# Kernel optimization log

Hardware: AMD Instinct MI355X
Metric: run time of the kernel (lower is better)

The kernel has to match this reference:

```python
import jax, jax.numpy as jnp
import numpy as np

B, T_OBS, T_FUT, D, H = 8192, 128, 64, 5, 128


def _gru_step(h, x, Wih, Whh, bih, bhh):
    # PyTorch GRU math, gate order (r, z, n) in the stacked [3H, *] weights.
    gi = x @ Wih.T + bih          # [B, 3H]
    gh = h @ Whh.T + bhh          # [B, 3H]
    ir, iz, inn = jnp.split(gi, 3, axis=-1)
    hr, hz, hn = jnp.split(gh, 3, axis=-1)
    r = jax.nn.sigmoid(ir + hr)
    z = jax.nn.sigmoid(iz + hz)
    n = jnp.tanh(inn + r * hn)
    return (1.0 - z) * n + z * h


def setup_inputs() -> dict:
    key = jax.random.key(0)
    ks = jax.random.split(key, 12)
    s = 0.1  # modest init scale to keep gates in a sane range
    return {
        "obs": jax.random.normal(ks[0], (B, T_OBS, D), jnp.float32),
        "target": jax.random.normal(ks[1], (B, T_FUT, D), jnp.float32),
        "enc_Wih": jax.random.normal(ks[2], (3 * H, D), jnp.float32) * s,
        "enc_Whh": jax.random.normal(ks[3], (3 * H, H), jnp.float32) * s,
        "enc_bih": jax.random.normal(ks[4], (3 * H,), jnp.float32) * s,
        "enc_bhh": jax.random.normal(ks[5], (3 * H,), jnp.float32) * s,
        "cell_Wih": jax.random.normal(ks[6], (3 * H, D), jnp.float32) * s,
        "cell_Whh": jax.random.normal(ks[7], (3 * H, H), jnp.float32) * s,
        "cell_bih": jax.random.normal(ks[8], (3 * H,), jnp.float32) * s,
        "cell_bhh": jax.random.normal(ks[9], (3 * H,), jnp.float32) * s,
        "head_W": jax.random.normal(ks[10], (D, H), jnp.float32) * s,
        "head_b": jax.random.normal(ks[11], (D,), jnp.float32) * s,
    }


def reference(obs, target, enc_Wih, enc_Whh, enc_bih, enc_bhh,
              cell_Wih, cell_Whh, cell_bih, cell_bhh, head_W, head_b):
    b = obs.shape[0]
    h0 = jnp.zeros((b, H), obs.dtype)

    # --- encoder: GRU over obs, keep only final hidden state ---
    def enc_step(h, x):
        h_new = _gru_step(h, x, enc_Wih, enc_Whh, enc_bih, enc_bhh)
        return h_new, None
    hT, _ = jax.lax.scan(enc_step, h0, jnp.swapaxes(obs, 0, 1))  # xs: [T_obs, B, D]

    # --- teacher-forced rollout: x_0 = obs[:, -1], x_t = target[:, t-1] ---
    xs = jnp.concatenate([obs[:, -1:, :], target[:, :-1, :]], axis=1)  # [B, T_fut, D]
    def roll_step(h, x):
        h_new = _gru_step(h, x, cell_Wih, cell_Whh, cell_bih, cell_bhh)
        return h_new, h_new
    _, hs = jax.lax.scan(roll_step, hT, jnp.swapaxes(xs, 0, 1))  # hs: [T_fut, B, H]

    preds = jnp.einsum('tbh,dh->tbd', hs, head_W) + head_b  # [T_fut, B, D]
    return jnp.swapaxes(preds, 0, 1)  # [B, T_fut, D]
```

## Files before the change

kernel.cpp:

```cpp
#include <hip/hip_runtime.h>

#define B_TOT 8192
#define T_OBS 128
#define T_FUT 64
#define T_ALL 192
#define DIN 5
#define HD 128
#define BT 32
#define LDSTR 136

#define LOG2E 1.44269504088896340736f

typedef __attribute__((ext_vector_type(8))) short short8;
typedef __attribute__((ext_vector_type(4))) float f32x4;
typedef __attribute__((ext_vector_type(2))) unsigned int u32x2;
typedef __attribute__((ext_vector_type(4))) unsigned int u32x4;

__device__ inline short f2bf(float f) {
    unsigned u = __float_as_uint(f);
    u += 0x7FFFu + ((u >> 16) & 1u);
    return (short)(u >> 16);
}

__device__ inline unsigned cvtpk(float lo, float hi) {
    unsigned r;
    asm volatile("v_cvt_pk_bf16_f32 %0, %1, %2" : "=v"(r) : "v"(lo), "v"(hi));
    return r;
}

__device__ inline f32x4 MFMA(short8 a, short8 b, f32x4 c) {
    return __builtin_amdgcn_mfma_f32_16x16x32_bf16(a, b, c, 0, 0, 0);
}

__device__ inline short8 load_w8s(const float* p, float s) {
    float4 a = *reinterpret_cast<const float4*>(p);
    float4 b = *reinterpret_cast<const float4*>(p + 4);
    short8 r;
    r[0] = f2bf(a.x * s); r[1] = f2bf(a.y * s); r[2] = f2bf(a.z * s); r[3] = f2bf(a.w * s);
    r[4] = f2bf(b.x * s); r[5] = f2bf(b.y * s); r[6] = f2bf(b.z * s); r[7] = f2bf(b.w * s);
    return r;
}
__device__ inline short8 load_w5s(const float* p, float s) {
    short8 r = (short8)0;
    r[0] = f2bf(p[0] * s); r[1] = f2bf(p[1] * s); r[2] = f2bf(p[2] * s);
    r[3] = f2bf(p[3] * s); r[4] = f2bf(p[4] * s);
    return r;
}

__global__ __launch_bounds__(512, 1)
void gru_tracemodel_kernel(const float* __restrict__ obs, const float* __restrict__ target,
                           const float* __restrict__ eWih, const float* __restrict__ eWhh,
                           const float* __restrict__ ebih, const float* __restrict__ ebhh,
                           const float* __restrict__ cWih, const float* __restrict__ cWhh,
                           const float* __restrict__ cbih, const float* __restrict__ cbhh,
                           const float* __restrict__ headW, const float* __restrict__ headb,
                           float* __restrict__ out)
{
    __shared__ __attribute__((aligned(16))) short Abuf[2][BT][LDSTR];

    const int tid   = threadIdx.x;
    const int wave  = tid >> 6;
    const int lane  = tid & 63;
    const int q     = lane >> 4;
    const int c     = lane & 15;
    const int b0    = blockIdx.x * BT;
    const int wbase = wave * 16;

    for (int i = tid; i < 2 * BT * LDSTR; i += 512) ((short*)Abuf)[i] = 0;

    short8 Wr[5], Wz[5], Wn[5];
    f32x4  br4, bz4, bnh4, bni4;

    auto load_phase = [&](const float* Wih, const float* Whh,
                          const float* bih, const float* bhh) {
        const int nr = 0 * HD + wbase + c;
        const int nz = 1 * HD + wbase + c;
        const int nn = 2 * HD + wbase + c;
        #pragma unroll
        for (int kt = 0; kt < 4; ++kt) {
            Wr[kt] = load_w8s(Whh + nr * HD + kt * 32 + q * 8, LOG2E);
            Wz[kt] = load_w8s(Whh + nz * HD + kt * 32 + q * 8, LOG2E);
            Wn[kt] = load_w8s(Whh + nn * HD + kt * 32 + q * 8, 2.f * LOG2E);
        }
        Wr[4] = (q == 0) ? load_w5s(Wih + nr * DIN, LOG2E) : (short8)0;
        Wz[4] = (q == 0) ? load_w5s(Wih + nz * DIN, LOG2E) : (short8)0;
        Wn[4] = (q == 0) ? load_w5s(Wih + nn * DIN, 2.f * LOG2E) : (short8)0;
        const int n0 = wbase + q * 4;
        #pragma unroll
        for (int r = 0; r < 4; ++r) {
            br4[r]  = (bih[0 * HD + n0 + r] + bhh[0 * HD + n0 + r]) * LOG2E;
            bz4[r]  = (bih[1 * HD + n0 + r] + bhh[1 * HD + n0 + r]) * LOG2E;
            bni4[r] = bih[2 * HD + n0 + r] * (2.f * LOG2E);
            bnh4[r] = bhh[2 * HD + n0 + r] * (2.f * LOG2E);
        }
    };
    load_phase(eWih, eWhh, ebih, ebhh);

    short8 Whd[4];
    f32x4  hb4;
    #pragma unroll
    for (int kt = 0; kt < 4; ++kt)
        Whd[kt] = (c < DIN) ? load_w8s(headW + c * HD + kt * 32 + q * 8, 1.f) : (short8)0;
    #pragma unroll
    for (int r = 0; r < 4; ++r)
        hb4[r] = (q * 4 + r < DIN) ? headb[q * 4 + r] : 0.f;

    float hreg[2][4] = {{0.f,0.f,0.f,0.f},{0.f,0.f,0.f,0.f}};

    const float* obsr[2] = { obs + (size_t)(b0 + c) * (T_OBS * DIN),
                             obs + (size_t)(b0 + 16 + c) * (T_OBS * DIN) };
    const float* tgtr[2] = { target + (size_t)(b0 + c) * (T_FUT * DIN),
                             target + (size_t)(b0 + 16 + c) * (T_FUT * DIN) };
    float x5[2][5] = {{0,0,0,0,0},{0,0,0,0,0}};
    if (q == 0) {
        #pragma unroll
        for (int a = 0; a < 2; ++a) {
            float4 v4 = *reinterpret_cast<const float4*>(obsr[a]);
            x5[a][0] = v4.x; x5[a][1] = v4.y; x5[a][2] = v4.z; x5[a][3] = v4.w;
            x5[a][4] = obsr[a][4];
        }
    }

#define GRU_STEP(T, DO_HEAD, ENC)                                              \
  {                                                                            \
    __syncthreads();                                                           \
    const int p_ = (T) & 1;                                                    \
    short8 ah[2][4];                                                           \
    _Pragma("unroll")                                                          \
    for (int a = 0; a < 2; ++a) {                                              \
      const short* ap = &Abuf[p_][a * 16 + c][0];                              \
      _Pragma("unroll")                                                        \
      for (int kt = 0; kt < 4; ++kt)                                           \
        ah[a][kt] = *reinterpret_cast<const short8*>(ap + kt * 32 + q * 8);    \
    }                                                                          \
    if (DO_HEAD) {                                                             \
      const int s_ = (T) - (T_OBS + 1);                                        \
      if (wave == (s_ & 7)) {                                                  \
        const int d0 = q * 4;                                                  \
        _Pragma("unroll")                                                      \
        for (int a = 0; a < 2; ++a) {                                          \
          f32x4 acc = hb4;                                                     \
          _Pragma("unroll")                                                    \
          for (int kt = 0; kt < 4; ++kt)                                       \
            acc = MFMA(Whd[kt], ah[a][kt], acc);                               \
          if (d0 < DIN) {                                                      \
            float* op = out + ((size_t)(b0 + a * 16 + c) * T_FUT + s_) * DIN + d0; \
            op[0] = acc[0];                                                    \
            if (q == 0) { op[1] = acc[1]; op[2] = acc[2]; op[3] = acc[3]; }    \
          }                                                                    \
        }                                                                      \
      }                                                                        \
    }                                                                          \
    short8 ax[2];                                                              \
    {                                                                          \
      u32x4 va = { cvtpk(x5[0][0], x5[0][1]), cvtpk(x5[0][2], x5[0][3]),       \
                   cvtpk(x5[0][4], 0.f), 0u };                                 \
      u32x4 vb = { cvtpk(x5[1][0], x5[1][1]), cvtpk(x5[1][2], x5[1][3]),       \
                   cvtpk(x5[1][4], 0.f), 0u };                                 \
      ax[0] = __builtin_bit_cast(short8, va);                                  \
      ax[1] = __builtin_bit_cast(short8, vb);                                  \
      if (q == 0) {                                                            \
        const int tn_ = (T) + 1;                                               \
        _Pragma("unroll")                                                      \
        for (int a = 0; a < 2; ++a) {                                          \
          const float* px = (ENC)                                              \
              ? (obsr[a] + ((tn_ < T_OBS) ? tn_ : (T_OBS - 1)) * DIN)          \
              : (tgtr[a] + (tn_ - T_OBS - 1) * DIN);                           \
          float4 v4 = *reinterpret_cast<const float4*>(px);                    \
          x5[a][0] = v4.x; x5[a][1] = v4.y; x5[a][2] = v4.z; x5[a][3] = v4.w;  \
          x5[a][4] = px[4];                                                    \
        }                                                                      \
      }                                                                        \
    }                                                                          \
    _Pragma("unroll")                                                          \
    for (int a = 0; a < 2; ++a) {                                              \
      f32x4 aR  = MFMA(Wr[0], ah[a][0], br4);                                  \
      f32x4 aZ  = MFMA(Wz[0], ah[a][0], bz4);                                  \
      f32x4 aNh = MFMA(Wn[0], ah[a][0], bnh4);                                 \
      _Pragma("unroll")                                                        \
      for (int kt = 1; kt < 4; ++kt) {                                         \
        aR  = MFMA(Wr[kt], ah[a][kt], aR);                                     \
        aZ  = MFMA(Wz[kt], ah[a][kt], aZ);                                     \
        aNh = MFMA(Wn[kt], ah[a][kt], aNh);                                    \
      }                                                                        \
      aR  = MFMA(Wr[4], ax[a], aR);                                            \
      aZ  = MFMA(Wz[4], ax[a], aZ);                                            \
      f32x4 aNi = MFMA(Wn[4], ax[a], bni4);                                    \
      float hn[4];                                                             \
      _Pragma("unroll")                                                        \
      for (int r = 0; r < 4; ++r) {                                            \
        float er  = __builtin_amdgcn_exp2f(-aR[r]);                            \
        float rv  = __builtin_amdgcn_rcpf(1.f + er);                           \
        float yv  = fmaf(rv, aNh[r], aNi[r]);                                  \
        float ey  = __builtin_amdgcn_exp2f(yv);                                \
        float ez  = __builtin_amdgcn_exp2f(-aZ[r]);                            \
        float d2  = 1.f + ey;                                                  \
        float d1  = 1.f + ez;                                                  \
        float em1 = ey - 1.f;                                                  \
        float num = fmaf(ez, em1, hreg[a][r] * d2);                            \
        float h_  = num * __builtin_amdgcn_rcpf(d1 * d2);                      \
        hreg[a][r] = h_;                                                       \
        hn[r] = h_;                                                            \
      }                                                                        \
      u32x2 wv = { cvtpk(hn[0], hn[1]), cvtpk(hn[2], hn[3]) };                 \
      *reinterpret_cast<u32x2*>(&Abuf[1 - p_][a * 16 + c][wbase + q * 4]) = wv;\
    }                                                                          \
  }

    for (int t = 0; t < T_OBS; ++t) GRU_STEP(t, 0, 1);

    load_phase(cWih, cWhh, cbih, cbhh);
    GRU_STEP(T_OBS, 0, 0);

    for (int t = T_OBS + 1; t < T_ALL; ++t) GRU_STEP(t, 1, 0);

    __syncthreads();
    if (wave == ((T_FUT - 1) & 7)) {
        const int p_ = T_ALL & 1;
        const int s_ = T_FUT - 1;
        const int d0 = q * 4;
        #pragma unroll
        for (int a = 0; a < 2; ++a) {
            const short* ap = &Abuf[p_][a * 16 + c][0];
            f32x4 acc = hb4;
            #pragma unroll
            for (int kt = 0; kt < 4; ++kt) {
                short8 h8 = *reinterpret_cast<const short8*>(ap + kt * 32 + q * 8);
                acc = MFMA(Whd[kt], h8, acc);
            }
            if (d0 < DIN) {
                float* op = out + ((size_t)(b0 + a * 16 + c) * T_FUT + s_) * DIN + d0;
                op[0] = acc[0];
                if (q == 0) { op[1] = acc[1]; op[2] = acc[2]; op[3] = acc[3]; }
            }
        }
    }
#undef GRU_STEP
}

extern "C" void kernel_launch(void* const* d_in, const int* in_sizes, int n_in,
                              void* d_out, int out_size, void* d_ws, size_t ws_size,
                              hipStream_t stream)
{
    (void)in_sizes; (void)n_in; (void)d_ws; (void)ws_size; (void)out_size;
    gru_tracemodel_kernel<<<dim3(B_TOT / BT), dim3(512), 0, stream>>>(
        (const float*)d_in[0],  (const float*)d_in[1],
        (const float*)d_in[2],  (const float*)d_in[3],
        (const float*)d_in[4],  (const float*)d_in[5],
        (const float*)d_in[6],  (const float*)d_in[7],
        (const float*)d_in[8],  (const float*)d_in[9],
        (const float*)d_in[10], (const float*)d_in[11],
        (float*)d_out);
}
```

Measured before the change: 322.5 us.

## Halve batch tile to 16 with 4 waves each owning 32 hidden units

Restructures the work split so each block handles 16 batch rows using 256 threads (4 waves), with each wave computing two 16-wide hidden-unit groups instead of two batch halves. This doubles the grid to 512 blocks and allows two blocks per CU, meant to improve latency hiding across the sequential recurrence and reduce barrier cost per block. The head weights move from registers into LDS to relieve register pressure for the doubled per-wave gate weights. The trade-off is that each thread now holds twice as many weight fragments in registers.

```diff
diff --git a/kernel.cpp b/kernel.cpp
--- a/kernel.cpp
+++ b/kernel.cpp
@@ -6,8 +6,9 @@
 #define T_ALL 192
 #define DIN 5
 #define HD 128
-#define BT 32
+#define BT 16
 #define LDSTR 136
+#define NTHR 256
 
 #define LOG2E 1.44269504088896340736f
 
@@ -47,7 +48,7 @@
     return r;
 }
 
-__global__ __launch_bounds__(512, 1)
+__global__ __launch_bounds__(NTHR, 2)
 void gru_tracemodel_kernel(const float* __restrict__ obs, const float* __restrict__ target,
                            const float* __restrict__ eWih, const float* __restrict__ eWhh,
                            const float* __restrict__ ebih, const float* __restrict__ ebhh,
@@ -57,135 +58,132 @@
                            float* __restrict__ out)
 {
     __shared__ __attribute__((aligned(16))) short Abuf[2][BT][LDSTR];
-
-    const int tid   = threadIdx.x;
-    const int wave  = tid >> 6;
-    const int lane  = tid & 63;
-    const int q     = lane >> 4;
-    const int c     = lane & 15;
-    const int b0    = blockIdx.x * BT;
-    const int wbase = wave * 16;
-
-    for (int i = tid; i < 2 * BT * LDSTR; i += 512) ((short*)Abuf)[i] = 0;
-
-    short8 Wr[5], Wz[5], Wn[5];
-    f32x4  br4, bz4, bnh4, bni4;
+    __shared__ __attribute__((aligned(16))) short Hw[DIN][LDSTR];
+    __shared__ float HbLds[8];
+
+    const int tid  = threadIdx.x;
+    const int wave = tid >> 6;
+    const int lane = tid & 63;
+    const int q    = lane >> 4;
+    const int c    = lane & 15;
+    const int b0   = blockIdx.x * BT;
+    const int wb0  = wave * 32;
+
+    for (int i = tid; i < 2 * BT * LDSTR; i += NTHR) ((short*)Abuf)[i] = 0;
+
+    short8 Wr[2][5], Wz[2][5], Wn[2][5];
+    f32x4  br4[2], bz4[2], bnh4[2], bni4[2];
 
     auto load_phase = [&](const float* Wih, const float* Whh,
                           const float* bih, const float* bhh) {
-        const int nr = 0 * HD + wbase + c;
-        const int nz = 1 * HD + wbase + c;
-        const int nn = 2 * HD + wbase + c;
+        #pragma unroll
+        for (int g = 0; g < 2; ++g) {
+            const int nr = 0 * HD + wb0 + 16 * g + c;
+            const int nz = 1 * HD + wb0 + 16 * g + c;
+            const int nn = 2 * HD + wb0 + 16 * g + c;
+            #pragma unroll
+            for (int kt = 0; kt < 4; ++kt) {
+                Wr[g][kt] = load_w8s(Whh + nr * HD + kt * 32 + q * 8, LOG2E);
+                Wz[g][kt] = load_w8s(Whh + nz * HD + kt * 32 + q * 8, LOG2E);
+                Wn[g][kt] = load_w8s(Whh + nn * HD + kt * 32 + q * 8, 2.f * LOG2E);
+            }
+            Wr[g][4] = (q == 0) ? load_w5s(Wih + nr * DIN, LOG2E) : (short8)0;
+            Wz[g][4] = (q == 0) ? load_w5s(Wih + nz * DIN, LOG2E) : (short8)0;
+            Wn[g][4] = (q == 0) ? load_w5s(Wih + nn * DIN, 2.f * LOG2E) : (short8)0;
+            const int n0 = wb0 + 16 * g + q * 4;
+            #pragma unroll
+            for (int r = 0; r < 4; ++r) {
+                br4[g][r]  = (bih[0 * HD + n0 + r] + bhh[0 * HD + n0 + r]) * LOG2E;
+                bz4[g][r]  = (bih[1 * HD + n0 + r] + bhh[1 * HD + n0 + r]) * LOG2E;
+                bni4[g][r] = bih[2 * HD + n0 + r] * (2.f * LOG2E);
+                bnh4[g][r] = bhh[2 * HD + n0 + r] * (2.f * LOG2E);
+            }
+        }
+    };
+    load_phase(eWih, eWhh, ebih, ebhh);
+
+    if (wave == 0 && c < DIN) {
         #pragma unroll
         for (int kt = 0; kt < 4; ++kt) {
-            Wr[kt] = load_w8s(Whh + nr * HD + kt * 32 + q * 8, LOG2E);
-            Wz[kt] = load_w8s(Whh + nz * HD + kt * 32 + q * 8, LOG2E);
-            Wn[kt] = load_w8s(Whh + nn * HD + kt * 32 + q * 8, 2.f * LOG2E);
-        }
-        Wr[4] = (q == 0) ? load_w5s(Wih + nr * DIN, LOG2E) : (short8)0;
-        Wz[4] = (q == 0) ? load_w5s(Wih + nz * DIN, LOG2E) : (short8)0;
-        Wn[4] = (q == 0) ? load_w5s(Wih + nn * DIN, 2.f * LOG2E) : (short8)0;
-        const int n0 = wbase + q * 4;
-        #pragma unroll
-        for (int r = 0; r < 4; ++r) {
-            br4[r]  = (bih[0 * HD + n0 + r] + bhh[0 * HD + n0 + r]) * LOG2E;
-            bz4[r]  = (bih[1 * HD + n0 + r] + bhh[1 * HD + n0 + r]) * LOG2E;
-            bni4[r] = bih[2 * HD + n0 + r] * (2.f * LOG2E);
-            bnh4[r] = bhh[2 * HD + n0 + r] * (2.f * LOG2E);
-        }
-    };
-    load_phase(eWih, eWhh, ebih, ebhh);
-
-    short8 Whd[4];
-    f32x4  hb4;
-    #pragma unroll
-    for (int kt = 0; kt < 4; ++kt)
-        Whd[kt] = (c < DIN) ? load_w8s(headW + c * HD + kt * 32 + q * 8, 1.f) : (short8)0;
-    #pragma unroll
-    for (int r = 0; r < 4; ++r)
-        hb4[r] = (q * 4 + r < DIN) ? headb[q * 4 + r] : 0.f;
+            short8 w = load_w8s(headW + c * HD + kt * 32 + q * 8, 1.f);
+            *reinterpret_cast<short8*>(&Hw[c][kt * 32 + q * 8]) = w;
+        }
+    }
+    if (tid < 8) HbLds[tid] = (tid < DIN) ? headb[tid] : 0.f;
 
     float hreg[2][4] = {{0.f,0.f,0.f,0.f},{0.f,0.f,0.f,0.f}};
 
-    const float* obsr[2] = { obs + (size_t)(b0 + c) * (T_OBS * DIN),
-                             obs + (size_t)(b0 + 16 + c) * (T_OBS * DIN) };
-    const float* tgtr[2] = { target + (size_t)(b0 + c) * (T_FUT * DIN),
-                             target + (size_t)(b0 + 16 + c) * (T_FUT * DIN) };
-    float x5[2][5] = {{0,0,0,0,0},{0,0,0,0,0}};
+    const float* obsr = obs    + (size_t)(b0 + c) * (T_OBS * DIN);
+    const float* tgtr = target + (size_t)(b0 + c) * (T_FUT * DIN);
+    float x5[5] = {0, 0, 0, 0, 0};
     if (q == 0) {
-        #pragma unroll
-        for (int a = 0; a < 2; ++a) {
-            float4 v4 = *reinterpret_cast<const float4*>(obsr[a]);
-            x5[a][0] = v4.x; x5[a][1] = v4.y; x5[a][2] = v4.z; x5[a][3] = v4.w;
-            x5[a][4] = obsr[a][4];
-        }
+        float4 v4 = *reinterpret_cast<const float4*>(obsr);
+        x5[0] = v4.x; x5[1] = v4.y; x5[2] = v4.z; x5[3] = v4.w;
+        x5[4] = obsr[4];
     }
 
 #define GRU_STEP(T, DO_HEAD, ENC)                                              \
   {                                                                            \
     __syncthreads();                                                           \
     const int p_ = (T) & 1;                                                    \
-    short8 ah[2][4];                                                           \
-    _Pragma("unroll")                                                          \
-    for (int a = 0; a < 2; ++a) {                                              \
-      const short* ap = &Abuf[p_][a * 16 + c][0];                              \
+    short8 ah[4];                                                              \
+    {                                                                          \
+      const short* ap = &Abuf[p_][c][0];                                       \
       _Pragma("unroll")                                                        \
       for (int kt = 0; kt < 4; ++kt)                                           \
-        ah[a][kt] = *reinterpret_cast<const short8*>(ap + kt * 32 + q * 8);    \
+        ah[kt] = *reinterpret_cast<const short8*>(ap + kt * 32 + q * 8);       \
     }                                                                          \
     if (DO_HEAD) {                                                             \
       const int s_ = (T) - (T_OBS + 1);                                        \
-      if (wave == (s_ & 7)) {                                                  \
+      if (wave == (s_ & 3)) {                                                  \
+        const short* hwp = &Hw[(c < DIN) ? c : 0][0];                          \
+        f32x4 acc = {0.f, 0.f, 0.f, 0.f};                                      \
+        _Pragma("unroll")                                                      \
+        for (int kt = 0; kt < 4; ++kt) {                                       \
+          short8 wh = *reinterpret_cast<const short8*>(hwp + kt * 32 + q * 8); \
+          acc = MFMA(wh, ah[kt], acc);                                         \
+        }                                                                      \
         const int d0 = q * 4;                                                  \
-        _Pragma("unroll")                                                      \
-        for (int a = 0; a < 2; ++a) {                                          \
-          f32x4 acc = hb4;                                                     \
-          _Pragma("unroll")                                                    \
-          for (int kt = 0; kt < 4; ++kt)                                       \
-            acc = MFMA(Whd[kt], ah[a][kt], acc);                               \
-          if (d0 < DIN) {                                                      \
-            float* op = out + ((size_t)(b0 + a * 16 + c) * T_FUT + s_) * DIN + d0; \
-            op[0] = acc[0];                                                    \
-            if (q == 0) { op[1] = acc[1]; op[2] = acc[2]; op[3] = acc[3]; }    \
+        if (d0 < DIN) {                                                        \
+          float* op = out + ((size_t)(b0 + c) * T_FUT + s_) * DIN + d0;        \
+          op[0] = acc[0] + HbLds[d0];                                          \
+          if (q == 0) {                                                        \
+            op[1] = acc[1] + HbLds[1];                                         \
+            op[2] = acc[2] + HbLds[2];                                         \
+            op[3] = acc[3] + HbLds[3];                                         \
           }                                                                    \
         }                                                                      \
       }                                                                        \
     }                                                                          \
-    short8 ax[2];                                                              \
+    short8 ax;                                                                 \
     {                                                                          \
-      u32x4 va = { cvtpk(x5[0][0], x5[0][1]), cvtpk(x5[0][2], x5[0][3]),       \
-                   cvtpk(x5[0][4], 0.f), 0u };                                 \
-      u32x4 vb = { cvtpk(x5[1][0], x5[1][1]), cvtpk(x5[1][2], x5[1][3]),       \
-                   cvtpk(x5[1][4], 0.f), 0u };                                 \
-      ax[0] = __builtin_bit_cast(short8, va);                                  \
-      ax[1] = __builtin_bit_cast(short8, vb);                                  \
+      u32x4 va = { cvtpk(x5[0], x5[1]), cvtpk(x5[2], x5[3]),                   \
+                   cvtpk(x5[4], 0.f), 0u };                                    \
+      ax = __builtin_bit_cast(short8, va);                                     \
       if (q == 0) {                                                            \
         const int tn_ = (T) + 1;                                               \
-        _Pragma("unroll")                                                      \
-        for (int a = 0; a < 2; ++a) {                                          \
-          const float* px = (ENC)                                              \
-              ? (obsr[a] + ((tn_ < T_OBS) ? tn_ : (T_OBS - 1)) * DIN)          \
-              : (tgtr[a] + (tn_ - T_OBS - 1) * DIN);                           \
-          float4 v4 = *reinterpret_cast<const float4*>(px);                    \
-          x5[a][0] = v4.x; x5[a][1] = v4.y; x5[a][2] = v4.z; x5[a][3] = v4.w;  \
-          x5[a][4] = px[4];                                                    \
-        }                                                                      \
+        const float* px = (ENC)                                                \
+            ? (obsr + ((tn_ < T_OBS) ? tn_ : (T_OBS - 1)) * DIN)               \
+            : (tgtr + (tn_ - T_OBS - 1) * DIN);                                \
+        float4 v4 = *reinterpret_cast<const float4*>(px);                      \
+        x5[0] = v4.x; x5[1] = v4.y; x5[2] = v4.z; x5[3] = v4.w;                \
+        x5[4] = px[4];                                                         \
       }                                                                        \
     }                                                                          \
     _Pragma("unroll")                                                          \
-    for (int a = 0; a < 2; ++a) {                                              \
-      f32x4 aR  = MFMA(Wr[0], ah[a][0], br4);                                  \
-      f32x4 aZ  = MFMA(Wz[0], ah[a][0], bz4);                                  \
-      f32x4 aNh = MFMA(Wn[0], ah[a][0], bnh4);                                 \
+    for (int g = 0; g < 2; ++g) {                                              \
+      f32x4 aR  = MFMA(Wr[g][0], ah[0], br4[g]);                               \
+      f32x4 aZ  = MFMA(Wz[g][0], ah[0], bz4[g]);                               \
+      f32x4 aNh = MFMA(Wn[g][0], ah[0], bnh4[g]);                              \
       _Pragma("unroll")                                                        \
       for (int kt = 1; kt < 4; ++kt) {                                         \
-        aR  = MFMA(Wr[kt], ah[a][kt], aR);                                     \
-        aZ  = MFMA(Wz[kt], ah[a][kt], aZ);                                     \
-        aNh = MFMA(Wn[kt], ah[a][kt], aNh);                                    \
-      }                                                                        \
-      aR  = MFMA(Wr[4], ax[a], aR);                                            \
-      aZ  = MFMA(Wz[4], ax[a], aZ);                                            \
-      f32x4 aNi = MFMA(Wn[4], ax[a], bni4);                                    \
+        aR  = MFMA(Wr[g][kt], ah[kt], aR);                                     \
+        aZ  = MFMA(Wz[g][kt], ah[kt], aZ);                                     \
+        aNh = MFMA(Wn[g][kt], ah[kt], aNh);                                    \
+      }                                                                        \
+      aR  = MFMA(Wr[g][4], ax, aR);                                            \
+      aZ  = MFMA(Wz[g][4], ax, aZ);                                            \
+      f32x4 aNi = MFMA(Wn[g][4], ax, bni4[g]);                                 \
       float hn[4];                                                             \
       _Pragma("unroll")                                                        \
       for (int r = 0; r < 4; ++r) {                                            \
@@ -197,13 +195,14 @@
         float d2  = 1.f + ey;                                                  \
         float d1  = 1.f + ez;                                                  \
         float em1 = ey - 1.f;                                                  \
-        float num = fmaf(ez, em1, hreg[a][r] * d2);                            \
+        float num = fmaf(ez, em1, hreg[g][r] * d2);                            \
         float h_  = num * __builtin_amdgcn_rcpf(d1 * d2);                      \
-        hreg[a][r] = h_;                                                       \
+        hreg[g][r] = h_;                                                       \
         hn[r] = h_;                                                            \
       }                                                                        \
       u32x2 wv = { cvtpk(hn[0], hn[1]), cvtpk(hn[2], hn[3]) };                 \
-      *reinterpret_cast<u32x2*>(&Abuf[1 - p_][a * 16 + c][wbase + q * 4]) = wv;\
+      *reinterpret_cast<u32x2*>(                                               \
+          &Abuf[1 - p_][c][wb0 + 16 * g + q * 4]) = wv;                        \
     }                                                                          \
   }
 
@@ -215,23 +214,26 @@
     for (int t = T_OBS + 1; t < T_ALL; ++t) GRU_STEP(t, 1, 0);
 
     __syncthreads();
-    if (wave == ((T_FUT - 1) & 7)) {
+    if (wave == ((T_FUT - 1) & 3)) {
         const int p_ = T_ALL & 1;
         const int s_ = T_FUT - 1;
         const int d0 = q * 4;
+        const short* ap  = &Abuf[p_][c][0];
+        const short* hwp = &Hw[(c < DIN) ? c : 0][0];
+        f32x4 acc = {0.f, 0.f, 0.f, 0.f};
         #pragma unroll
-        for (int a = 0; a < 2; ++a) {
-            const short* ap = &Abuf[p_][a * 16 + c][0];
-            f32x4 acc = hb4;
-            #pragma unroll
-            for (int kt = 0; kt < 4; ++kt) {
-                short8 h8 = *reinterpret_cast<const short8*>(ap + kt * 32 + q * 8);
-                acc = MFMA(Whd[kt], h8, acc);
-            }
-            if (d0 < DIN) {
-                float* op = out + ((size_t)(b0 + a * 16 + c) * T_FUT + s_) * DIN + d0;
-                op[0] = acc[0];
-                if (q == 0) { op[1] = acc[1]; op[2] = acc[2]; op[3] = acc[3]; }
+        for (int kt = 0; kt < 4; ++kt) {
+            short8 h8 = *reinterpret_cast<const short8*>(ap + kt * 32 + q * 8);
+            short8 wh = *reinterpret_cast<const short8*>(hwp + kt * 32 + q * 8);
+            acc = MFMA(wh, h8, acc);
+        }
+        if (d0 < DIN) {
+            float* op = out + ((size_t)(b0 + c) * T_FUT + s_) * DIN + d0;
+            op[0] = acc[0] + HbLds[d0];
+            if (q == 0) {
+                op[1] = acc[1] + HbLds[1];
+                op[2] = acc[2] + HbLds[2];
+                op[3] = acc[3] + HbLds[3];
             }
         }
     }
@@ -243,7 +245,7 @@
                               hipStream_t stream)
 {
     (void)in_sizes; (void)n_in; (void)d_ws; (void)ws_size; (void)out_size;
-    gru_tracemodel_kernel<<<dim3(B_TOT / BT), dim3(512), 0, stream>>>(
+    gru_tracemodel_kernel<<<dim3(B_TOT / BT), dim3(NTHR), 0, stream>>>(
         (const float*)d_in[0],  (const float*)d_in[1],
         (const float*)d_in[2],  (const float*)d_in[3],
         (const float*)d_in[4],  (const float*)d_in[5],
```

Result: slower. 377.0 us (+16.9%).
